# Kernel tuning notes

Hardware: AMD Instinct MI355X
Metric: run time of the kernel (lower is better)

## Reference

```python
import jax, jax.numpy as jnp
import numpy as np

NEG_INF = -1e30

def masked_softmax(logits, mask, axis):
    # mask broadcastable to logits; 1 = keep, 0 = mask out
    masked = jnp.where(mask > 0, logits, NEG_INF)
    return jax.nn.softmax(masked, axis=axis)

def setup_inputs() -> dict:
    key = jax.random.key(0)
    ks = jax.random.split(key, 6)
    B, H, C, Q = 64, 128, 1024, 128
    c = jax.random.normal(ks[0], (B, H, C), dtype=jnp.float32)
    q = jax.random.normal(ks[1], (B, H, Q), dtype=jnp.float32)
    c_mask = jnp.ones((B, C), dtype=jnp.float32)
    q_mask = jnp.ones((B, Q), dtype=jnp.float32)
    # xavier_uniform for (H,1): bound = sqrt(6/(H+1))
    bnd_v = float(np.sqrt(6.0 / (H + 1)))
    context_weights = jax.random.uniform(ks[2], (H, 1), minval=-bnd_v, maxval=bnd_v, dtype=jnp.float32)
    query_weights = jax.random.uniform(ks[3], (H, 1), minval=-bnd_v, maxval=bnd_v, dtype=jnp.float32)
    # xavier_uniform for (1,1,H): fan_in=1, fan_out=H -> bound = sqrt(6/(1+H))
    cq_weights = jax.random.uniform(ks[4], (1, 1, H), minval=-bnd_v, maxval=bnd_v, dtype=jnp.float32)
    bias = jnp.zeros((1,), dtype=jnp.float32)
    return {"c": c, "q": q, "c_mask": c_mask, "q_mask": q_mask,
            "context_weights": context_weights, "query_weights": query_weights,
            "cq_weights": cq_weights, "bias": bias}

def reference(c, q, c_mask, q_mask, context_weights, query_weights, cq_weights, bias):
    # to (B, len, H)
    c = jnp.swapaxes(c, 1, 2)  # (B, c_len, H)
    q = jnp.swapaxes(q, 1, 2)  # (B, q_len, H)
    B, c_len, H = c.shape
    q_len = q.shape[1]
    # trilinear similarity: (B, c_len, q_len)
    s0 = c @ context_weights                         # (B, c_len, 1)
    s1 = jnp.swapaxes(q @ query_weights, 1, 2)       # (B, 1, q_len)
    s2 = jnp.einsum('bch,bqh->bcq', c * cq_weights, q)
    S = s0 + s1 + s2 + bias
    a_att = masked_softmax(S, q_mask[:, None, :], axis=2)  # softmax over q_len
    b_att = masked_softmax(S, c_mask[:, :, None], axis=1)  # softmax over c_len
    a = jnp.einsum('bcq,bqh->bch', a_att, q)
    b = jnp.einsum('bcq,bkq,bkh->bch', a_att, b_att, c)
    x = jnp.concatenate([c, a, c * a, c * b], axis=2)  # (B, c_len, 4H)
    return jnp.swapaxes(x, 1, 2)  # (B, 4H, c_len)
```

## Files before the change

### kernel.cpp

```cpp
#include <hip/hip_runtime.h>
#include <math.h>

#define NEG_HUGE -1e30f
constexpr int B_ = 64, H_ = 128, C_ = 1024, Q_ = 128;

typedef __bf16 bf16x8 __attribute__((ext_vector_type(8)));
typedef float f32x4 __attribute__((ext_vector_type(4)));
typedef short short8 __attribute__((ext_vector_type(8)));
typedef short short4s __attribute__((ext_vector_type(4)));

__device__ __forceinline__ float bs2f(short s) {
  unsigned u = ((unsigned)(unsigned short)s) << 16;
  float f; __builtin_memcpy(&f, &u, 4); return f;
}
__device__ __forceinline__ short f2bs(float f) {
  unsigned u; __builtin_memcpy(&u, &f, 4);
  u = (u + 0x7fffu + ((u >> 16) & 1u)) >> 16;
  return (short)u;
}
__device__ __forceinline__ void nts4(float* p, float4 v) {
  f32x4 x; x[0] = v.x; x[1] = v.y; x[2] = v.z; x[3] = v.w;
  __builtin_nontemporal_store(x, (f32x4*)p);
}

__global__ __launch_bounds__(256) void kTc(const float* __restrict__ cin,
                                           const float* __restrict__ ctxw,
                                           short* __restrict__ cT,
                                           float* __restrict__ s0p) {
  __shared__ float T[64 * 69];
  const int t = threadIdx.x;
  const int c0 = blockIdx.x * 64, h0 = blockIdx.y * 64, b = blockIdx.z;
  {
    const int row = t >> 2, off = t & 3;
    const float* src = cin + (b * H_ + h0 + row) * C_ + c0;
#pragma unroll
    for (int j = 0; j < 4; ++j) {
      float4 v = *(const float4*)&src[off * 16 + j * 4];
      int cbase = off * 16 + j * 4;
      T[row * 69 + cbase + 0] = v.x;
      T[row * 69 + cbase + 1] = v.y;
      T[row * 69 + cbase + 2] = v.z;
      T[row * 69 + cbase + 3] = v.w;
    }
  }
  __syncthreads();
  {
    const int c = t >> 2, offh = t & 3;
    short* dst = cT + (b * C_ + c0 + c) * H_ + h0;
#pragma unroll
    for (int j = 0; j < 4; ++j) {
      int hs = offh * 16 + j * 4;
      short4s v;
      v[0] = f2bs(T[(hs + 0) * 69 + c]);
      v[1] = f2bs(T[(hs + 1) * 69 + c]);
      v[2] = f2bs(T[(hs + 2) * 69 + c]);
      v[3] = f2bs(T[(hs + 3) * 69 + c]);
      *(short4s*)&dst[hs] = v;
    }
  }
  if (t < 64) {
    float acc = 0.f;
#pragma unroll 8
    for (int h = 0; h < 64; ++h) acc += T[h * 69 + t] * ctxw[h0 + h];
    s0p[blockIdx.y * (B_ * C_) + b * C_ + c0 + t] = acc;
  }
}

__global__ __launch_bounds__(256) void kq(const float* __restrict__ qin,
                                          const float* __restrict__ qw,
                                          const float* __restrict__ cqw,
                                          const float* __restrict__ qmask,
                                          short* __restrict__ qTw,
                                          short* __restrict__ qbf,
                                          float* __restrict__ s1m) {
  __shared__ float T[64 * 130];
  const int t = threadIdx.x;
  const int q0 = blockIdx.x * 64, b = blockIdx.y;
#pragma unroll
  for (int p = 0; p < 8; ++p) {
    int fidx = t + 256 * p;
    int h = fidx >> 4, seg = fidx & 15;
    float4 v = *(const float4*)&qin[(b * H_ + h) * Q_ + q0 + seg * 4];
    T[(seg * 4 + 0) * 130 + h] = v.x;
    T[(seg * 4 + 1) * 130 + h] = v.y;
    T[(seg * 4 + 2) * 130 + h] = v.z;
    T[(seg * 4 + 3) * 130 + h] = v.w;
    short4s o; o[0] = f2bs(v.x); o[1] = f2bs(v.y); o[2] = f2bs(v.z); o[3] = f2bs(v.w);
    *(short4s*)&qbf[(b * H_ + h) * Q_ + q0 + seg * 4] = o;
  }
  __syncthreads();
  if (t < 64) {
    float acc = 0.f;
#pragma unroll 8
    for (int h = 0; h < 128; ++h) acc += T[t * 130 + h] * qw[h];
    float qm = (qmask[b * Q_ + q0 + t] > 0.f) ? 0.f : NEG_HUGE;
    s1m[b * Q_ + q0 + t] = acc + qm;
  }
  {
    const int q = t >> 2, off = t & 3;
    short* dst = qTw + (b * Q_ + q0 + q) * H_;
#pragma unroll
    for (int j = 0; j < 4; ++j) {
      int hbv = off * 32 + j * 8;
      short8 v;
#pragma unroll
      for (int i = 0; i < 8; ++i) v[i] = f2bs(T[q * 130 + hbv + i] * cqw[hbv + i]);
      *(short8*)&dst[hbv] = v;
    }
  }
}

__global__ __launch_bounds__(256) void k1_mfma(
    const short* __restrict__ cT, const short* __restrict__ qTw,
    const float* __restrict__ s1m, const float* __restrict__ cmask,
    const float* __restrict__ s0p,
    short* __restrict__ a_att, short* __restrict__ ePT,
    float* __restrict__ pcm, float* __restrict__ pcs) {
  __shared__ __align__(16) char uni[34816];
  __shared__ float s1mL[128], scolL[128], pw[512], mpL[128];
  short* AL = (short*)uni;
  short* BL = (short*)(uni + 10240);
  short* RP = (short*)uni;

  const int t = threadIdx.x;
  const int w = t >> 6, l = t & 63, quad = l >> 4, lcol = l & 15;
  const int bx = blockIdx.x, b = blockIdx.y, c0 = bx * 128;

  if (t < 128) {
    s1mL[t] = s1m[b * Q_ + t];
    float cm = (cmask[b * C_ + c0 + t] > 0.f) ? 0.f : NEG_HUGE;
    scolL[t] = cm + s0p[b * C_ + c0 + t] + s0p[B_ * C_ + b * C_ + c0 + t];
  }

  f32x4 acc[2][8];
#pragma unroll
  for (int mt = 0; mt < 2; ++mt)
#pragma unroll
    for (int nt = 0; nt < 8; ++nt) acc[mt][nt] = (f32x4){0.f, 0.f, 0.f, 0.f};

  const int ar = t >> 2, aoff = t & 3;

  for (int kc = 0; kc < 4; ++kc) {
    const int h0 = kc * 32;
    *(short8*)&AL[ar * 40 + aoff * 8] =
        *(const short8*)&cT[(b * C_ + c0 + ar) * H_ + h0 + aoff * 8];
    *(short8*)&AL[(64 + ar) * 40 + aoff * 8] =
        *(const short8*)&cT[(b * C_ + c0 + 64 + ar) * H_ + h0 + aoff * 8];
    *(short8*)&BL[ar * 40 + aoff * 8] =
        *(const short8*)&qTw[(b * Q_ + ar) * H_ + h0 + aoff * 8];
    *(short8*)&BL[(64 + ar) * 40 + aoff * 8] =
        *(const short8*)&qTw[(b * Q_ + 64 + ar) * H_ + h0 + aoff * 8];
    __syncthreads();
    bf16x8 af0 = *(bf16x8*)&AL[(w * 32 + lcol) * 40 + quad * 8];
    bf16x8 af1 = *(bf16x8*)&AL[(w * 32 + 16 + lcol) * 40 + quad * 8];
#pragma unroll
    for (int nt = 0; nt < 8; ++nt) {
      bf16x8 bfrag = *(bf16x8*)&BL[(nt * 16 + lcol) * 40 + quad * 8];
      acc[0][nt] = __builtin_amdgcn_mfma_f32_16x16x32_bf16(af0, bfrag, acc[0][nt], 0, 0, 0);
      acc[1][nt] = __builtin_amdgcn_mfma_f32_16x16x32_bf16(af1, bfrag, acc[1][nt], 0, 0, 0);
    }
    __syncthreads();
  }

  float s1v[8];
#pragma unroll
  for (int nt = 0; nt < 8; ++nt) s1v[nt] = s1mL[nt * 16 + lcol];
  float cs0[2][4];
#pragma unroll
  for (int mt = 0; mt < 2; ++mt)
#pragma unroll
    for (int r = 0; r < 4; ++r)
      cs0[mt][r] = scolL[w * 32 + mt * 16 + quad * 4 + r];

  float rm[2][4];
#pragma unroll
  for (int mt = 0; mt < 2; ++mt)
#pragma unroll
    for (int r = 0; r < 4; ++r) {
      float m = -INFINITY;
#pragma unroll
      for (int nt = 0; nt < 8; ++nt) m = fmaxf(m, acc[mt][nt][r] + s1v[nt]);
      rm[mt][r] = m;
    }
#pragma unroll
  for (int d = 1; d <= 8; d <<= 1)
#pragma unroll
    for (int mt = 0; mt < 2; ++mt)
#pragma unroll
      for (int r = 0; r < 4; ++r)
        rm[mt][r] = fmaxf(rm[mt][r], __shfl_xor(rm[mt][r], d));

  float pmv[8];
#pragma unroll
  for (int nt = 0; nt < 8; ++nt) {
    float m = -INFINITY;
#pragma unroll
    for (int mt = 0; mt < 2; ++mt)
#pragma unroll
      for (int r = 0; r < 4; ++r) m = fmaxf(m, acc[mt][nt][r] + cs0[mt][r]);
    pmv[nt] = m;
  }
#pragma unroll
  for (int nt = 0; nt < 8; ++nt) {
    pmv[nt] = fmaxf(pmv[nt], __shfl_xor(pmv[nt], 16));
    pmv[nt] = fmaxf(pmv[nt], __shfl_xor(pmv[nt], 32));
  }
  if (l < 16) {
#pragma unroll
    for (int nt = 0; nt < 8; ++nt) pw[w * 128 + nt * 16 + lcol] = pmv[nt];
  }

#pragma unroll
  for (int mt = 0; mt < 2; ++mt)
#pragma unroll
    for (int nt = 0; nt < 8; ++nt)
#pragma unroll
      for (int r = 0; r < 4; ++r)
        acc[mt][nt][r] = __expf(acc[mt][nt][r] + s1v[nt] - rm[mt][r]);

  float inv[2][4];
#pragma unroll
  for (int mt = 0; mt < 2; ++mt)
#pragma unroll
    for (int r = 0; r < 4; ++r) {
      float s = 0.f;
#pragma unroll
      for (int nt = 0; nt < 8; ++nt) s += acc[mt][nt][r];
      inv[mt][r] = s;
    }
#pragma unroll
  for (int d = 1; d <= 8; d <<= 1)
#pragma unroll
    for (int mt = 0; mt < 2; ++mt)
#pragma unroll
      for (int r = 0; r < 4; ++r)
        inv[mt][r] += __shfl_xor(inv[mt][r], d);
#pragma unroll
  for (int mt = 0; mt < 2; ++mt)
#pragma unroll
    for (int r = 0; r < 4; ++r) inv[mt][r] = 1.f / inv[mt][r];

#pragma unroll
  for (int mt = 0; mt < 2; ++mt)
#pragma unroll
    for (int nt = 0; nt < 8; ++nt)
#pragma unroll
      for (int r = 0; r < 4; ++r) {
        int row = w * 32 + mt * 16 + quad * 4 + r;
        int col = nt * 16 + lcol;
        RP[row * 136 + col] = f2bs(acc[mt][nt][r] * inv[mt][r]);
      }
  __syncthreads();
  {
    const int row = t >> 1, half = t & 1;
    short* dst = a_att + (b * C_ + c0 + row) * Q_ + half * 64;
    const short* srcp = RP + row * 136 + half * 64;
#pragma unroll
    for (int j = 0; j < 8; ++j) *(short8*)&dst[j * 8] = *(const short8*)&srcp[j * 8];
  }
  __syncthreads();
  if (t < 128) {
    float m = fmaxf(fmaxf(pw[t], pw[128 + t]), fmaxf(pw[256 + t], pw[384 + t]));
    mpL[t] = m;
    pcm[(b * 8 + bx) * Q_ + t] = m;
  }
  __syncthreads();
  float mpv[8];
#pragma unroll
  for (int nt = 0; nt < 8; ++nt) mpv[nt] = mpL[nt * 16 + lcol];

  float crm[2][4];
#pragma unroll
  for (int mt = 0; mt < 2; ++mt)
#pragma unroll
    for (int r = 0; r < 4; ++r) crm[mt][r] = cs0[mt][r] + rm[mt][r];
  float psv[8];
#pragma unroll
  for (int nt = 0; nt < 8; ++nt) {
    const float sm = s1v[nt] + mpv[nt];
    const int qq = nt * 16 + lcol;
    float s = 0.f;
#pragma unroll
    for (int mt = 0; mt < 2; ++mt)
#pragma unroll
      for (int r = 0; r < 4; ++r) {
        float v = acc[mt][nt][r] * __expf(crm[mt][r] - sm);
        s += v;
        RP[qq * 136 + (w * 32 + mt * 16 + quad * 4 + r)] = f2bs(v);
      }
    psv[nt] = s;
  }
#pragma unroll
  for (int nt = 0; nt < 8; ++nt) {
    psv[nt] += __shfl_xor(psv[nt], 16);
    psv[nt] += __shfl_xor(psv[nt], 32);
  }
  if (l < 16) {
#pragma unroll
    for (int nt = 0; nt < 8; ++nt) pw[w * 128 + nt * 16 + lcol] = psv[nt];
  }
  __syncthreads();
  if (t < 128) pcs[(b * 8 + bx) * Q_ + t] = pw[t] + pw[128 + t] + pw[256 + t] + pw[384 + t];
  {
    const int qq = t >> 1, half = t & 1;
    short* dst = ePT + (b * Q_ + qq) * C_ + c0 + half * 64;
    const short* srcp = RP + qq * 136 + half * 64;
#pragma unroll
    for (int j = 0; j < 8; ++j) *(short8*)&dst[j * 8] = *(const short8*)&srcp[j * 8];
  }
}

__global__ __launch_bounds__(256) void k3_T(
    const short* __restrict__ ePT, const float* __restrict__ cin,
    const float* __restrict__ pcm, const float* __restrict__ pcs,
    float* __restrict__ Tpart) {
  __shared__ __align__(16) char uni[34816];
  short* AL = (short*)uni;
  short* BL = (short*)(uni + 10240);
  float* RPF = (float*)uni;
  __shared__ float scA[2][128];
  __shared__ float icL[128];
  const int t = threadIdx.x;
  const int w = t >> 6, l = t & 63, quad = l >> 4, lcol = l & 15;
  const int hb = blockIdx.x * 64, kc = blockIdx.y, b = blockIdx.z;

  if (t < 128) {
    float m[8]; float M = -INFINITY;
#pragma unroll
    for (int k = 0; k < 8; ++k) { m[k] = pcm[(b * 8 + k) * Q_ + t]; M = fmaxf(M, m[k]); }
    float s = 0.f;
#pragma unroll
    for (int k = 0; k < 8; ++k) s += pcs[(b * 8 + k) * Q_ + t] * __expf(m[k] - M);
    icL[t] = 1.f / s;
    scA[0][t] = __expf(m[kc * 2 + 0] - M);
    scA[1][t] = __expf(m[kc * 2 + 1] - M);
  }

  f32x4 acc[2][4];
#pragma unroll
  for (int mt = 0; mt < 2; ++mt)
#pragma unroll
    for (int nt = 0; nt < 4; ++nt) acc[mt][nt] = (f32x4){0.f, 0.f, 0.f, 0.f};

  const int ar = t >> 2, aoff = t & 3;
  __syncthreads();
  const float s00 = scA[0][ar], s01 = scA[0][64 + ar];
  const float s10 = scA[1][ar], s11 = scA[1][64 + ar];

  for (int ck = 0; ck < 8; ++ck) {
    const int coff = kc * 256 + ck * 32;
    const float sA0 = (ck < 4) ? s00 : s10;
    const float sA1 = (ck < 4) ? s01 : s11;
    {
      short8 v0 = *(const short8*)&ePT[(b * Q_ + ar) * C_ + coff + aoff * 8];
      short8 v1 = *(const short8*)&ePT[(b * Q_ + 64 + ar) * C_ + coff + aoff * 8];
      short8 o0, o1;
#pragma unroll
      for (int i = 0; i < 8; ++i) {
        o0[i] = f2bs(bs2f(v0[i]) * sA0);
        o1[i] = f2bs(bs2f(v1[i]) * sA1);
      }
      *(short8*)&AL[ar * 40 + aoff * 8] = o0;
      *(short8*)&AL[(64 + ar) * 40 + aoff * 8] = o1;
    }
    {
      const float* srcp = cin + (b * H_ + hb + ar) * C_ + coff + aoff * 8;
      short8 o;
#pragma unroll
      for (int i = 0; i < 8; ++i) o[i] = f2bs(srcp[i]);
      *(short8*)&BL[ar * 40 + aoff * 8] = o;
    }
    __syncthreads();
    bf16x8 af0 = *(bf16x8*)&AL[(w * 32 + lcol) * 40 + quad * 8];
    bf16x8 af1 = *(bf16x8*)&AL[(w * 32 + 16 + lcol) * 40 + quad * 8];
#pragma unroll
    for (int nt = 0; nt < 4; ++nt) {
      bf16x8 bfrag = *(bf16x8*)&BL[(nt * 16 + lcol) * 40 + quad * 8];
      acc[0][nt] = __builtin_amdgcn_mfma_f32_16x16x32_bf16(af0, bfrag, acc[0][nt], 0, 0, 0);
      acc[1][nt] = __builtin_amdgcn_mfma_f32_16x16x32_bf16(af1, bfrag, acc[1][nt], 0, 0, 0);
    }
    __syncthreads();
  }
#pragma unroll
  for (int mt = 0; mt < 2; ++mt)
#pragma unroll
    for (int nt = 0; nt < 4; ++nt)
#pragma unroll
      for (int r = 0; r < 4; ++r)
        RPF[(nt * 16 + lcol) * 136 + (w * 32 + mt * 16 + quad * 4 + r)] = acc[mt][nt][r];
  __syncthreads();
  {
    float* Tp = Tpart + (size_t)kc * (B_ * H_ * Q_) + ((size_t)b * H_ + hb) * Q_;
    const int lr = t >> 5, coln = (t & 31) * 4;
    float4 ic = *(const float4*)&icL[coln];
#pragma unroll
    for (int iter = 0; iter < 8; ++iter) {
      int hl = iter * 8 + lr;
      float4 v = *(float4*)&RPF[hl * 136 + coln];
      v.x *= ic.x; v.y *= ic.y; v.z *= ic.z; v.w *= ic.w;
      *(float4*)&Tp[hl * Q_ + coln] = v;
    }
  }
}

__global__ __launch_bounds__(256) void k3b(const float* __restrict__ Tpart,
                                           short* __restrict__ TmT) {
  const int gid = blockIdx.x * 256 + threadIdx.x;
  const int e = gid * 4;
  float4 s = make_float4(0.f, 0.f, 0.f, 0.f);
#pragma unroll
  for (int k = 0; k < 4; ++k) {
    float4 v = *(const float4*)&Tpart[(size_t)k * (B_ * H_ * Q_) + e];
    s.x += v.x; s.y += v.y; s.z += v.z; s.w += v.w;
  }
  short4s o;
  o[0] = f2bs(s.x); o[1] = f2bs(s.y); o[2] = f2bs(s.z); o[3] = f2bs(s.w);
  *(short4s*)&TmT[e] = o;
}

__global__ __launch_bounds__(256) void k4_out(
    const short* __restrict__ a_att, const short* __restrict__ qbf,
    const short* __restrict__ TmT, const float* __restrict__ cin,
    float* __restrict__ out) {
  __shared__ __align__(16) char uni[34816];
  short* AL = (short*)uni;
  short* B1 = (short*)(uni + 10240);
  short* B2 = (short*)(uni + 15360);
  float* RPF = (float*)uni;
  const int t = threadIdx.x;
  const int w = t >> 6, l = t & 63, quad = l >> 4, lcol = l & 15;
  const int c0 = blockIdx.x * 128, hb = blockIdx.y * 64, b = blockIdx.z;

  f32x4 accA[2][4], accB[2][4];
#pragma unroll
  for (int mt = 0; mt < 2; ++mt)
#pragma unroll
    for (int nt = 0; nt < 4; ++nt) {
      accA[mt][nt] = (f32x4){0.f, 0.f, 0.f, 0.f};
      accB[mt][nt] = (f32x4){0.f, 0.f, 0.f, 0.f};
    }

  const int ar = t >> 2, aoff = t & 3;
  for (int kc = 0; kc < 4; ++kc) {
    const int q0 = kc * 32;
    *(short8*)&AL[ar * 40 + aoff * 8] =
        *(const short8*)&a_att[(b * C_ + c0 + ar) * Q_ + q0 + aoff * 8];
    *(short8*)&AL[(64 + ar) * 40 + aoff * 8] =
        *(const short8*)&a_att[(b * C_ + c0 + 64 + ar) * Q_ + q0 + aoff * 8];
    *(short8*)&B1[ar * 40 + aoff * 8] =
        *(const short8*)&qbf[(b * H_ + hb + ar) * Q_ + q0 + aoff * 8];
    *(short8*)&B2[ar * 40 + aoff * 8] =
        *(const short8*)&TmT[(b * H_ + hb + ar) * Q_ + q0 + aoff * 8];
    __syncthreads();
    bf16x8 af0 = *(bf16x8*)&AL[(w * 32 + lcol) * 40 + quad * 8];
    bf16x8 af1 = *(bf16x8*)&AL[(w * 32 + 16 + lcol) * 40 + quad * 8];
#pragma unroll
    for (int nt = 0; nt < 4; ++nt) {
      bf16x8 bq = *(bf16x8*)&B1[(nt * 16 + lcol) * 40 + quad * 8];
      bf16x8 bt = *(bf16x8*)&B2[(nt * 16 + lcol) * 40 + quad * 8];
      accA[0][nt] = __builtin_amdgcn_mfma_f32_16x16x32_bf16(af0, bq, accA[0][nt], 0, 0, 0);
      accA[1][nt] = __builtin_amdgcn_mfma_f32_16x16x32_bf16(af1, bq, accA[1][nt], 0, 0, 0);
      accB[0][nt] = __builtin_amdgcn_mfma_f32_16x16x32_bf16(af0, bt, accB[0][nt], 0, 0, 0);
      accB[1][nt] = __builtin_amdgcn_mfma_f32_16x16x32_bf16(af1, bt, accB[1][nt], 0, 0, 0);
    }
    __syncthreads();
  }

  const int lr = t >> 5, coln = (t & 31) * 4;
  float* ob = out + (size_t)b * 512 * 1024;
  float4 cvv[8];

#pragma unroll
  for (int mt = 0; mt < 2; ++mt)
#pragma unroll
    for (int nt = 0; nt < 4; ++nt)
#pragma unroll
      for (int r = 0; r < 4; ++r)
        RPF[(nt * 16 + lcol) * 136 + (w * 32 + mt * 16 + quad * 4 + r)] = accA[mt][nt][r];
  __syncthreads();
#pragma unroll
  for (int iter = 0; iter < 8; ++iter) {
    int hl = iter * 8 + lr;
    int hrow = hb + hl;
    float4 la = *(float4*)&RPF[hl * 136 + coln];
    float4 cv = *(const float4*)&cin[(b * H_ + hrow) * C_ + c0 + coln];
    cvv[iter] = cv;
    nts4(&ob[(size_t)hrow * 1024 + c0 + coln], cv);
    nts4(&ob[(size_t)(128 + hrow) * 1024 + c0 + coln], la);
    float4 p = make_float4(cv.x * la.x, cv.y * la.y, cv.z * la.z, cv.w * la.w);
    nts4(&ob[(size_t)(256 + hrow) * 1024 + c0 + coln], p);
  }
  __syncthreads();
#pragma unroll
  for (int mt = 0; mt < 2; ++mt)
#pragma unroll
    for (int nt = 0; nt < 4; ++nt)
#pragma unroll
      for (int r = 0; r < 4; ++r)
        RPF[(nt * 16 + lcol) * 136 + (w * 32 + mt * 16 + quad * 4 + r)] = accB[mt][nt][r];
  __syncthreads();
#pragma unroll
  for (int iter = 0; iter < 8; ++iter) {
    int hl = iter * 8 + lr;
    int hrow = hb + hl;
    float4 lb = *(float4*)&RPF[hl * 136 + coln];
    float4 cv = cvv[iter];
    float4 p = make_float4(cv.x * lb.x, cv.y * lb.y, cv.z * lb.z, cv.w * lb.w);
    nts4(&ob[(size_t)(384 + hrow) * 1024 + c0 + coln], p);
  }
}

extern "C" void kernel_launch(void* const* d_in, const int* in_sizes, int n_in,
                              void* d_out, int out_size, void* d_ws, size_t ws_size,
                              hipStream_t stream) {
  const float* c     = (const float*)d_in[0];
  const float* q     = (const float*)d_in[1];
  const float* cmask = (const float*)d_in[2];
  const float* qmask = (const float*)d_in[3];
  const float* ctxw  = (const float*)d_in[4];
  const float* qw    = (const float*)d_in[5];
  const float* cqw   = (const float*)d_in[6];
  float* out = (float*)d_out;

  char* ws = (char*)d_ws;
  short* cT     = (short*)(ws);
  float* Tpart  = (float*)(ws);
  short* qTw    = (short*)(ws + 16777216);
  short* TmT    = (short*)(ws + 16777216);
  short* qbf    = (short*)(ws + 18874368);
  short* a_att  = (short*)(ws + 20971520);
  short* ePT    = (short*)(ws + 37748736);
  float* s0p    = (float*)(ws + 54525952);
  float* s1m    = (float*)(ws + 55050240);
  float* pcm    = (float*)(ws + 55083008);
  float* pcs    = (float*)(ws + 55345152);

  kTc<<<dim3(16, 2, B_), dim3(256), 0, stream>>>(c, ctxw, cT, s0p);
  kq<<<dim3(2, B_), dim3(256), 0, stream>>>(q, qw, cqw, qmask, qTw, qbf, s1m);
  k1_mfma<<<dim3(8, B_), dim3(256), 0, stream>>>(cT, qTw, s1m, cmask, s0p,
                                                 a_att, ePT, pcm, pcs);
  k3_T<<<dim3(2, 4, B_), dim3(256), 0, stream>>>(ePT, c, pcm, pcs, Tpart);
  k3b<<<dim3(1024), dim3(256), 0, stream>>>(Tpart, TmT);
  k4_out<<<dim3(8, 2, B_), dim3(256), 0, stream>>>(a_att, qbf, TmT, c, out);
}
```

Measured before the change: 238.7 us.

## Fuse c transpose into k1, drop split-K reduction in k3, swizzle LDS

Removes the separate kernel that transposed c to bf16 and computed s0. k1 now reads fp32 c directly, converts it, and accumulates the context-weight dot product while staging the full 128-wide H slab into XOR-swizzled LDS, so the GEMM runs with no per-chunk syncs. k3 is reorganised so each block covers all of C for a 16-row H slice and writes bf16 TmT directly, which eliminates the Tpart partials and the k3b reduction kernel. Grid orders are changed to put batch on x. The costs are 64KB of LDS in k1, which may limit occupancy, and strided global reads of c.

```diff
diff --git a/kernel.cpp b/kernel.cpp
--- a/kernel.cpp
+++ b/kernel.cpp
@@ -21,49 +21,6 @@
 __device__ __forceinline__ void nts4(float* p, float4 v) {
   f32x4 x; x[0] = v.x; x[1] = v.y; x[2] = v.z; x[3] = v.w;
   __builtin_nontemporal_store(x, (f32x4*)p);
-}
-
-__global__ __launch_bounds__(256) void kTc(const float* __restrict__ cin,
-                                           const float* __restrict__ ctxw,
-                                           short* __restrict__ cT,
-                                           float* __restrict__ s0p) {
-  __shared__ float T[64 * 69];
-  const int t = threadIdx.x;
-  const int c0 = blockIdx.x * 64, h0 = blockIdx.y * 64, b = blockIdx.z;
-  {
-    const int row = t >> 2, off = t & 3;
-    const float* src = cin + (b * H_ + h0 + row) * C_ + c0;
-#pragma unroll
-    for (int j = 0; j < 4; ++j) {
-      float4 v = *(const float4*)&src[off * 16 + j * 4];
-      int cbase = off * 16 + j * 4;
-      T[row * 69 + cbase + 0] = v.x;
-      T[row * 69 + cbase + 1] = v.y;
-      T[row * 69 + cbase + 2] = v.z;
-      T[row * 69 + cbase + 3] = v.w;
-    }
-  }
-  __syncthreads();
-  {
-    const int c = t >> 2, offh = t & 3;
-    short* dst = cT + (b * C_ + c0 + c) * H_ + h0;
-#pragma unroll
-    for (int j = 0; j < 4; ++j) {
-      int hs = offh * 16 + j * 4;
-      short4s v;
-      v[0] = f2bs(T[(hs + 0) * 69 + c]);
-      v[1] = f2bs(T[(hs + 1) * 69 + c]);
-      v[2] = f2bs(T[(hs + 2) * 69 + c]);
-      v[3] = f2bs(T[(hs + 3) * 69 + c]);
-      *(short4s*)&dst[hs] = v;
-    }
-  }
-  if (t < 64) {
-    float acc = 0.f;
-#pragma unroll 8
-    for (int h = 0; h < 64; ++h) acc += T[h * 69 + t] * ctxw[h0 + h];
-    s0p[blockIdx.y * (B_ * C_) + b * C_ + c0 + t] = acc;
-  }
 }
 
 __global__ __launch_bounds__(256) void kq(const float* __restrict__ qin,
@@ -111,25 +68,54 @@
 }
 
 __global__ __launch_bounds__(256) void k1_mfma(
-    const short* __restrict__ cT, const short* __restrict__ qTw,
+    const float* __restrict__ cin, const short* __restrict__ qTw,
     const float* __restrict__ s1m, const float* __restrict__ cmask,
-    const float* __restrict__ s0p,
+    const float* __restrict__ ctxw,
     short* __restrict__ a_att, short* __restrict__ ePT,
     float* __restrict__ pcm, float* __restrict__ pcs) {
-  __shared__ __align__(16) char uni[34816];
-  __shared__ float s1mL[128], scolL[128], pw[512], mpL[128];
+  __shared__ __align__(16) char uni[65536];
   short* AL = (short*)uni;
-  short* BL = (short*)(uni + 10240);
+  short* BL = (short*)(uni + 32768);
   short* RP = (short*)uni;
+  __shared__ float s1mL[128], scolL[128], pw[512], mpL[128], s0part[2][128];
 
   const int t = threadIdx.x;
   const int w = t >> 6, l = t & 63, quad = l >> 4, lcol = l & 15;
-  const int bx = blockIdx.x, b = blockIdx.y, c0 = bx * 128;
-
+  const int b = blockIdx.x, bx = blockIdx.y, c0 = bx * 128;
+
+  if (t < 128) s1mL[t] = s1m[b * Q_ + t];
+
+  {
+    const int cl = t & 127, hw = t >> 7;
+    float s0c = 0.f;
+#pragma unroll
+    for (int it = 0; it < 8; ++it) {
+      const int hb = hw + it * 2;
+      const float* sp = cin + ((size_t)(b * H_ + hb * 8)) * C_ + c0 + cl;
+      short8 o;
+#pragma unroll
+      for (int i = 0; i < 8; ++i) {
+        float f = sp[(size_t)i * C_];
+        o[i] = f2bs(f);
+        s0c += f * ctxw[hb * 8 + i];
+      }
+      *(short8*)&AL[cl * 128 + 8 * (hb ^ (cl & 7))] = o;
+    }
+    s0part[hw][cl] = s0c;
+  }
+  {
+    const int q = t >> 1, hb0 = (t & 1) * 8;
+#pragma unroll
+    for (int i = 0; i < 8; ++i) {
+      const int hb = hb0 + i;
+      *(short8*)&BL[q * 128 + 8 * (hb ^ (q & 7))] =
+          *(const short8*)&qTw[(b * Q_ + q) * H_ + hb * 8];
+    }
+  }
+  __syncthreads();
   if (t < 128) {
-    s1mL[t] = s1m[b * Q_ + t];
     float cm = (cmask[b * C_ + c0 + t] > 0.f) ? 0.f : NEG_HUGE;
-    scolL[t] = cm + s0p[b * C_ + c0 + t] + s0p[B_ * C_ + b * C_ + c0 + t];
+    scolL[t] = cm + s0part[0][t] + s0part[1][t];
   }
 
   f32x4 acc[2][8];
@@ -138,29 +124,20 @@
 #pragma unroll
     for (int nt = 0; nt < 8; ++nt) acc[mt][nt] = (f32x4){0.f, 0.f, 0.f, 0.f};
 
-  const int ar = t >> 2, aoff = t & 3;
-
+#pragma unroll
   for (int kc = 0; kc < 4; ++kc) {
-    const int h0 = kc * 32;
-    *(short8*)&AL[ar * 40 + aoff * 8] =
-        *(const short8*)&cT[(b * C_ + c0 + ar) * H_ + h0 + aoff * 8];
-    *(short8*)&AL[(64 + ar) * 40 + aoff * 8] =
-        *(const short8*)&cT[(b * C_ + c0 + 64 + ar) * H_ + h0 + aoff * 8];
-    *(short8*)&BL[ar * 40 + aoff * 8] =
-        *(const short8*)&qTw[(b * Q_ + ar) * H_ + h0 + aoff * 8];
-    *(short8*)&BL[(64 + ar) * 40 + aoff * 8] =
-        *(const short8*)&qTw[(b * Q_ + 64 + ar) * H_ + h0 + aoff * 8];
-    __syncthreads();
-    bf16x8 af0 = *(bf16x8*)&AL[(w * 32 + lcol) * 40 + quad * 8];
-    bf16x8 af1 = *(bf16x8*)&AL[(w * 32 + 16 + lcol) * 40 + quad * 8];
+    const int kb = kc * 4 + quad;
+    const int sw = 8 * (kb ^ (lcol & 7));
+    bf16x8 af0 = *(bf16x8*)&AL[(w * 32 + lcol) * 128 + sw];
+    bf16x8 af1 = *(bf16x8*)&AL[(w * 32 + 16 + lcol) * 128 + sw];
 #pragma unroll
     for (int nt = 0; nt < 8; ++nt) {
-      bf16x8 bfrag = *(bf16x8*)&BL[(nt * 16 + lcol) * 40 + quad * 8];
+      bf16x8 bfrag = *(bf16x8*)&BL[(nt * 16 + lcol) * 128 + sw];
       acc[0][nt] = __builtin_amdgcn_mfma_f32_16x16x32_bf16(af0, bfrag, acc[0][nt], 0, 0, 0);
       acc[1][nt] = __builtin_amdgcn_mfma_f32_16x16x32_bf16(af1, bfrag, acc[1][nt], 0, 0, 0);
     }
-    __syncthreads();
-  }
+  }
+  __syncthreads();
 
   float s1v[8];
 #pragma unroll
@@ -313,16 +290,16 @@
 __global__ __launch_bounds__(256) void k3_T(
     const short* __restrict__ ePT, const float* __restrict__ cin,
     const float* __restrict__ pcm, const float* __restrict__ pcs,
-    float* __restrict__ Tpart) {
-  __shared__ __align__(16) char uni[34816];
+    short* __restrict__ TmT) {
+  __shared__ __align__(16) char uni[36864];
   short* AL = (short*)uni;
-  short* BL = (short*)(uni + 10240);
+  short* BL = (short*)(uni + 32768);
   float* RPF = (float*)uni;
-  __shared__ float scA[2][128];
+  __shared__ float scT[8][128];
   __shared__ float icL[128];
   const int t = threadIdx.x;
   const int w = t >> 6, l = t & 63, quad = l >> 4, lcol = l & 15;
-  const int hb = blockIdx.x * 64, kc = blockIdx.y, b = blockIdx.z;
+  const int b = blockIdx.x, hs = blockIdx.y;
 
   if (t < 128) {
     float m[8]; float M = -INFINITY;
@@ -330,92 +307,68 @@
     for (int k = 0; k < 8; ++k) { m[k] = pcm[(b * 8 + k) * Q_ + t]; M = fmaxf(M, m[k]); }
     float s = 0.f;
 #pragma unroll
-    for (int k = 0; k < 8; ++k) s += pcs[(b * 8 + k) * Q_ + t] * __expf(m[k] - M);
+    for (int k = 0; k < 8; ++k) {
+      float e = __expf(m[k] - M);
+      scT[k][t] = e;
+      s += pcs[(b * 8 + k) * Q_ + t] * e;
+    }
     icL[t] = 1.f / s;
-    scA[0][t] = __expf(m[kc * 2 + 0] - M);
-    scA[1][t] = __expf(m[kc * 2 + 1] - M);
-  }
-
-  f32x4 acc[2][4];
-#pragma unroll
-  for (int mt = 0; mt < 2; ++mt)
-#pragma unroll
-    for (int nt = 0; nt < 4; ++nt) acc[mt][nt] = (f32x4){0.f, 0.f, 0.f, 0.f};
-
-  const int ar = t >> 2, aoff = t & 3;
-  __syncthreads();
-  const float s00 = scA[0][ar], s01 = scA[0][64 + ar];
-  const float s10 = scA[1][ar], s11 = scA[1][64 + ar];
+  }
+
+  f32x4 acc[2];
+  acc[0] = (f32x4){0.f, 0.f, 0.f, 0.f};
+  acc[1] = (f32x4){0.f, 0.f, 0.f, 0.f};
+
+  const int q = t >> 1, cb0 = (t & 1) * 8;
+  const int h = t >> 4, co2 = (t & 15) * 8;
+  __syncthreads();
 
   for (int ck = 0; ck < 8; ++ck) {
-    const int coff = kc * 256 + ck * 32;
-    const float sA0 = (ck < 4) ? s00 : s10;
-    const float sA1 = (ck < 4) ? s01 : s11;
+    const float sA = scT[ck][q];
+#pragma unroll
+    for (int i = 0; i < 8; ++i) {
+      const int cb = cb0 + i;
+      short8 v = *(const short8*)&ePT[(b * Q_ + q) * C_ + ck * 128 + cb * 8];
+      short8 o;
+#pragma unroll
+      for (int j = 0; j < 8; ++j) o[j] = f2bs(bs2f(v[j]) * sA);
+      *(short8*)&AL[q * 128 + 8 * (cb ^ (q & 7))] = o;
+    }
     {
-      short8 v0 = *(const short8*)&ePT[(b * Q_ + ar) * C_ + coff + aoff * 8];
-      short8 v1 = *(const short8*)&ePT[(b * Q_ + 64 + ar) * C_ + coff + aoff * 8];
-      short8 o0, o1;
-#pragma unroll
-      for (int i = 0; i < 8; ++i) {
-        o0[i] = f2bs(bs2f(v0[i]) * sA0);
-        o1[i] = f2bs(bs2f(v1[i]) * sA1);
-      }
-      *(short8*)&AL[ar * 40 + aoff * 8] = o0;
-      *(short8*)&AL[(64 + ar) * 40 + aoff * 8] = o1;
-    }
-    {
-      const float* srcp = cin + (b * H_ + hb + ar) * C_ + coff + aoff * 8;
+      const float* sp = cin + ((size_t)(b * H_ + hs * 16 + h)) * C_ + ck * 128 + co2;
+      float4 v0 = *(const float4*)&sp[0];
+      float4 v1 = *(const float4*)&sp[4];
       short8 o;
-#pragma unroll
-      for (int i = 0; i < 8; ++i) o[i] = f2bs(srcp[i]);
-      *(short8*)&BL[ar * 40 + aoff * 8] = o;
+      o[0] = f2bs(v0.x); o[1] = f2bs(v0.y); o[2] = f2bs(v0.z); o[3] = f2bs(v0.w);
+      o[4] = f2bs(v1.x); o[5] = f2bs(v1.y); o[6] = f2bs(v1.z); o[7] = f2bs(v1.w);
+      *(short8*)&BL[h * 128 + 8 * ((co2 >> 3) ^ (h & 7))] = o;
     }
     __syncthreads();
-    bf16x8 af0 = *(bf16x8*)&AL[(w * 32 + lcol) * 40 + quad * 8];
-    bf16x8 af1 = *(bf16x8*)&AL[(w * 32 + 16 + lcol) * 40 + quad * 8];
-#pragma unroll
-    for (int nt = 0; nt < 4; ++nt) {
-      bf16x8 bfrag = *(bf16x8*)&BL[(nt * 16 + lcol) * 40 + quad * 8];
-      acc[0][nt] = __builtin_amdgcn_mfma_f32_16x16x32_bf16(af0, bfrag, acc[0][nt], 0, 0, 0);
-      acc[1][nt] = __builtin_amdgcn_mfma_f32_16x16x32_bf16(af1, bfrag, acc[1][nt], 0, 0, 0);
+#pragma unroll
+    for (int ks = 0; ks < 4; ++ks) {
+      const int kb = ks * 4 + quad;
+      const int sw = 8 * (kb ^ (lcol & 7));
+      bf16x8 bfrag = *(bf16x8*)&BL[lcol * 128 + sw];
+      bf16x8 af0 = *(bf16x8*)&AL[(w * 32 + lcol) * 128 + sw];
+      bf16x8 af1 = *(bf16x8*)&AL[(w * 32 + 16 + lcol) * 128 + sw];
+      acc[0] = __builtin_amdgcn_mfma_f32_16x16x32_bf16(af0, bfrag, acc[0], 0, 0, 0);
+      acc[1] = __builtin_amdgcn_mfma_f32_16x16x32_bf16(af1, bfrag, acc[1], 0, 0, 0);
     }
     __syncthreads();
   }
 #pragma unroll
   for (int mt = 0; mt < 2; ++mt)
 #pragma unroll
-    for (int nt = 0; nt < 4; ++nt)
-#pragma unroll
-      for (int r = 0; r < 4; ++r)
-        RPF[(nt * 16 + lcol) * 136 + (w * 32 + mt * 16 + quad * 4 + r)] = acc[mt][nt][r];
-  __syncthreads();
-  {
-    float* Tp = Tpart + (size_t)kc * (B_ * H_ * Q_) + ((size_t)b * H_ + hb) * Q_;
-    const int lr = t >> 5, coln = (t & 31) * 4;
-    float4 ic = *(const float4*)&icL[coln];
-#pragma unroll
-    for (int iter = 0; iter < 8; ++iter) {
-      int hl = iter * 8 + lr;
-      float4 v = *(float4*)&RPF[hl * 136 + coln];
-      v.x *= ic.x; v.y *= ic.y; v.z *= ic.z; v.w *= ic.w;
-      *(float4*)&Tp[hl * Q_ + coln] = v;
-    }
-  }
-}
-
-__global__ __launch_bounds__(256) void k3b(const float* __restrict__ Tpart,
-                                           short* __restrict__ TmT) {
-  const int gid = blockIdx.x * 256 + threadIdx.x;
-  const int e = gid * 4;
-  float4 s = make_float4(0.f, 0.f, 0.f, 0.f);
-#pragma unroll
-  for (int k = 0; k < 4; ++k) {
-    float4 v = *(const float4*)&Tpart[(size_t)k * (B_ * H_ * Q_) + e];
-    s.x += v.x; s.y += v.y; s.z += v.z; s.w += v.w;
-  }
-  short4s o;
-  o[0] = f2bs(s.x); o[1] = f2bs(s.y); o[2] = f2bs(s.z); o[3] = f2bs(s.w);
-  *(short4s*)&TmT[e] = o;
+    for (int r = 0; r < 4; ++r)
+      RPF[lcol * 136 + (w * 32 + mt * 16 + quad * 4 + r)] = acc[mt][r];
+  __syncthreads();
+  {
+    const int hh = t >> 4, qo = (t & 15) * 8;
+    short8 o;
+#pragma unroll
+    for (int i = 0; i < 8; ++i) o[i] = f2bs(RPF[hh * 136 + qo + i] * icL[qo + i]);
+    *(short8*)&TmT[(b * H_ + hs * 16 + hh) * Q_ + qo] = o;
+  }
 }
 
 __global__ __launch_bounds__(256) void k4_out(
@@ -429,7 +382,7 @@
   float* RPF = (float*)uni;
   const int t = threadIdx.x;
   const int w = t >> 6, l = t & 63, quad = l >> 4, lcol = l & 15;
-  const int c0 = blockIdx.x * 128, hb = blockIdx.y * 64, b = blockIdx.z;
+  const int b = blockIdx.x, hb = blockIdx.y * 64, c0 = blockIdx.z * 128;
 
   f32x4 accA[2][4], accB[2][4];
 #pragma unroll
@@ -523,23 +476,18 @@
   float* out = (float*)d_out;
 
   char* ws = (char*)d_ws;
-  short* cT     = (short*)(ws);
-  float* Tpart  = (float*)(ws);
-  short* qTw    = (short*)(ws + 16777216);
-  short* TmT    = (short*)(ws + 16777216);
-  short* qbf    = (short*)(ws + 18874368);
-  short* a_att  = (short*)(ws + 20971520);
-  short* ePT    = (short*)(ws + 37748736);
-  float* s0p    = (float*)(ws + 54525952);
-  float* s1m    = (float*)(ws + 55050240);
-  float* pcm    = (float*)(ws + 55083008);
-  float* pcs    = (float*)(ws + 55345152);
-
-  kTc<<<dim3(16, 2, B_), dim3(256), 0, stream>>>(c, ctxw, cT, s0p);
+  short* qTw    = (short*)(ws);
+  short* qbf    = (short*)(ws + 2097152);
+  short* a_att  = (short*)(ws + 4194304);
+  short* ePT    = (short*)(ws + 20971520);
+  short* TmT    = (short*)(ws + 37748736);
+  float* s1m    = (float*)(ws + 39845888);
+  float* pcm    = (float*)(ws + 39878656);
+  float* pcs    = (float*)(ws + 40140800);
+
   kq<<<dim3(2, B_), dim3(256), 0, stream>>>(q, qw, cqw, qmask, qTw, qbf, s1m);
-  k1_mfma<<<dim3(8, B_), dim3(256), 0, stream>>>(cT, qTw, s1m, cmask, s0p,
+  k1_mfma<<<dim3(B_, 8), dim3(256), 0, stream>>>(c, qTw, s1m, cmask, ctxw,
                                                  a_att, ePT, pcm, pcs);
-  k3_T<<<dim3(2, 4, B_), dim3(256), 0, stream>>>(ePT, c, pcm, pcs, Tpart);
-  k3b<<<dim3(1024), dim3(256), 0, stream>>>(Tpart, TmT);
-  k4_out<<<dim3(8, 2, B_), dim3(256), 0, stream>>>(a_att, qbf, TmT, c, out);
-}
+  k3_T<<<dim3(B_, 8), dim3(256), 0, stream>>>(ePT, c, pcm, pcs, TmT);
+  k4_out<<<dim3(B_, 2, 8), dim3(256), 0, stream>>>(a_att, qbf, TmT, c, out);
+}
```

After: 241.7 us. Within noise of the previous version (+1.2%).
